# Kernel optimization log

Hardware: AMD Instinct MI355X
Metric: run time of the kernel (lower is better)

Reference implementation:

```python
import jax, jax.numpy as jnp
import numpy as np

FRAME_LENGTH = 2048
HOP_LENGTH = 512


def setup_inputs() -> dict:
    key = jax.random.key(0)
    # (batch, num_channels, samples): 8 clips, stereo, 30 s @ 16 kHz
    x = jax.random.normal(key, (8, 2, 480000), dtype=jnp.float32)
    return {"x": x}


def reference(x):
    """Faithful Enframe.forward.

    The original applies a Conv1d whose weight is the identity matrix
    torch.eye(FL)[:, None, :] with stride=hop, per channel, then concatenates
    channel results along dim=1. Mathematically out[b, n*FL + k, t] =
    x[b, n, t*hop + k]. We implement it as a strided gather (the efficient
    form of the same math).
    """
    B, C, S = x.shape
    FL, HOP = FRAME_LENGTH, HOP_LENGTH
    T = (S - FL) // HOP + 1  # frames_num = 934 for S=480000
    # gather_idx[k, t] = t*HOP + k  -> (FL, T)
    gather_idx = jnp.arange(FL)[:, None] + jnp.arange(T)[None, :] * HOP
    frames = x[:, :, gather_idx]  # (B, C, FL, T)
    # torch.cat over channel dim puts channel-major blocks of size FL on dim 1
    return frames.reshape(B, C * FL, T)
```

## Files before the change

kernel.cpp:

```cpp
#include <hip/hip_runtime.h>


constexpr int FL  = 2048;
constexpr int HOP = 512;
constexpr int TT  = 64;
constexpr int RT  = 64;
constexpr int ROWS = TT + 3;
constexpr int LSTR = RT + 1;

__global__ __launch_bounds__(256)
void enframe_kernel(const float* __restrict__ x, float* __restrict__ out,
                    int S, int T) {
    __shared__ float lds[ROWS * LSTR];

    const int bc = blockIdx.x;
    const int t0 = blockIdx.y * TT;
    const int r0 = blockIdx.z * RT;
    const int tid = threadIdx.x;

    {
        const int rg   = tid & 15;
        const int row0 = tid >> 4;
        const float* xb = x + (size_t)bc * S;
#pragma unroll
        for (int p = 0; p < 5; ++p) {
            const int row = p * 16 + row0;
            if (row < ROWS) {
                const size_t base = (size_t)(t0 + row) * HOP + r0;
                if (base + RT <= (size_t)S) {
                    const float4 v = *(const float4*)(xb + base + rg * 4);
                    float* l = lds + row * LSTR + rg * 4;
                    l[0] = v.x; l[1] = v.y; l[2] = v.z; l[3] = v.w;
                }
            }
        }
    }
    __syncthreads();

    const int tg = tid & 15;
    const int ko = tid >> 4;
    const int tl = tg * 4;
    const int t  = t0 + tl;
    float* ob = out + (size_t)bc * FL * T;
    const bool full = (t + 3 < T);
#pragma unroll
    for (int rb = 0; rb < RT; rb += 16) {
        const int rr = rb + ko;
        const int kb = r0 + rr;
#pragma unroll
        for (int h = 0; h < 4; ++h) {
            const int k = h * HOP + kb;
            const float* l = lds + (tl + h) * LSTR + rr;
            if (full) {
                float4 v = { l[0 * LSTR], l[1 * LSTR], l[2 * LSTR], l[3 * LSTR] };
                *(float4*)(ob + (size_t)k * T + t) = v;
            } else {
#pragma unroll
                for (int j = 0; j < 4; ++j)
                    if (t + j < T) ob[(size_t)k * T + t + j] = l[j * LSTR];
            }
        }
    }
}

extern "C" void kernel_launch(void* const* d_in, const int* in_sizes, int n_in,
                              void* d_out, int out_size, void* d_ws, size_t ws_size,
                              hipStream_t stream) {
    const float* x = (const float*)d_in[0];
    float* out = (float*)d_out;
    const int BC = 16;
    const int S  = in_sizes[0] / BC;
    const int T  = (S - FL) / HOP + 1;
    const int t_tiles = (T + TT - 1) / TT;
    const int r_tiles = HOP / RT;
    dim3 grid(BC, (unsigned)t_tiles, (unsigned)r_tiles);
    enframe_kernel<<<grid, 256, 0, stream>>>(x, out, S, T);
}
```

Before: 152.5 us.

## Loop each block over time chunks with register-prefetched next tile

Restructures the enframe kernel into a persistent-style loop. Each block now handles a 16-row slice of the hop and half of all time chunks, instead of one 64x64 tile. The next chunk's input is prefetched into registers while the current chunk is written out from LDS, overlapping loads with stores. The grid shrinks to 16x32x2 blocks, so fewer blocks are resident, and each thread issues a single narrow 16-float load row. This trades launch parallelism for fewer blocks and less redundant overlap-row loading per tile.

```diff
diff --git a/kernel.cpp b/kernel.cpp
--- a/kernel.cpp
+++ b/kernel.cpp
@@ -1,10 +1,10 @@
 #include <hip/hip_runtime.h>
 
 
-constexpr int FL  = 2048;
-constexpr int HOP = 512;
-constexpr int TT  = 64;
-constexpr int RT  = 64;
+constexpr int FL   = 2048;
+constexpr int HOP  = 512;
+constexpr int RT   = 16;
+constexpr int TT   = 64;
 constexpr int ROWS = TT + 3;
 constexpr int LSTR = RT + 1;
 
@@ -14,50 +14,73 @@
     __shared__ float lds[ROWS * LSTR];
 
     const int bc = blockIdx.x;
-    const int t0 = blockIdx.y * TT;
-    const int r0 = blockIdx.z * RT;
+    const int r0 = blockIdx.y * RT;
+    const int th = blockIdx.z;
+    const int nch  = (T + TT - 1) / TT;
+    const int half = (nch + 1) / 2;
+    const int c_begin = th * half;
+    const int c_end   = th ? nch : half;
+
     const int tid = threadIdx.x;
+    const float* xb = x + (size_t)bc * S;
+    float* ob = out + (size_t)bc * FL * T;
+    const int max_row = S / HOP - 1;
 
+    const int lrow = tid >> 2;
+    const int lrg  = (tid & 3) * 4;
+    const bool tail = tid < (ROWS - 64) * 4;
+    const int trow2 = 64 + (tid >> 2);
+
+    float4 a0 = {0,0,0,0}, a1 = {0,0,0,0};
     {
-        const int rg   = tid & 15;
-        const int row0 = tid >> 4;
-        const float* xb = x + (size_t)bc * S;
-#pragma unroll
-        for (int p = 0; p < 5; ++p) {
-            const int row = p * 16 + row0;
-            if (row < ROWS) {
-                const size_t base = (size_t)(t0 + row) * HOP + r0;
-                if (base + RT <= (size_t)S) {
-                    const float4 v = *(const float4*)(xb + base + rg * 4);
-                    float* l = lds + row * LSTR + rg * 4;
-                    l[0] = v.x; l[1] = v.y; l[2] = v.z; l[3] = v.w;
-                }
+        const int t0 = c_begin * TT;
+        const int tr = t0 + lrow;
+        if (tr <= max_row) a0 = *(const float4*)(xb + (size_t)tr * HOP + r0 + lrg);
+        if (tail) {
+            const int tr2 = t0 + trow2;
+            if (tr2 <= max_row) a1 = *(const float4*)(xb + (size_t)tr2 * HOP + r0 + lrg);
+        }
+    }
+
+    for (int c = c_begin; c < c_end; ++c) {
+        if (c > c_begin) __syncthreads();
+        {
+            float* l = lds + lrow * LSTR + lrg;
+            l[0] = a0.x; l[1] = a0.y; l[2] = a0.z; l[3] = a0.w;
+            if (tail) {
+                float* l2 = lds + trow2 * LSTR + lrg;
+                l2[0] = a1.x; l2[1] = a1.y; l2[2] = a1.z; l2[3] = a1.w;
             }
         }
-    }
-    __syncthreads();
+        __syncthreads();
 
-    const int tg = tid & 15;
-    const int ko = tid >> 4;
-    const int tl = tg * 4;
-    const int t  = t0 + tl;
-    float* ob = out + (size_t)bc * FL * T;
-    const bool full = (t + 3 < T);
-#pragma unroll
-    for (int rb = 0; rb < RT; rb += 16) {
-        const int rr = rb + ko;
-        const int kb = r0 + rr;
+        if (c + 1 < c_end) {
+            const int t0n = (c + 1) * TT;
+            const int tr = t0n + lrow;
+            a0 = (tr <= max_row) ? *(const float4*)(xb + (size_t)tr * HOP + r0 + lrg)
+                                 : float4{0,0,0,0};
+            if (tail) {
+                const int tr2 = t0n + trow2;
+                a1 = (tr2 <= max_row) ? *(const float4*)(xb + (size_t)tr2 * HOP + r0 + lrg)
+                                      : float4{0,0,0,0};
+            }
+        }
+
+        const int t0 = c * TT;
+        const int r  = tid >> 4;
+        const int tl = (tid & 15) * 4;
+        const bool full = (t0 + TT <= T);
 #pragma unroll
         for (int h = 0; h < 4; ++h) {
-            const int k = h * HOP + kb;
-            const float* l = lds + (tl + h) * LSTR + rr;
+            const float* l = lds + (tl + h) * LSTR + r;
+            float* op = ob + (size_t)(h * HOP + r0 + r) * T + t0 + tl;
             if (full) {
-                float4 v = { l[0 * LSTR], l[1 * LSTR], l[2 * LSTR], l[3 * LSTR] };
-                *(float4*)(ob + (size_t)k * T + t) = v;
+                float4 v = { l[0], l[LSTR], l[2 * LSTR], l[3 * LSTR] };
+                *(float4*)op = v;
             } else {
 #pragma unroll
                 for (int j = 0; j < 4; ++j)
-                    if (t + j < T) ob[(size_t)k * T + t + j] = l[j * LSTR];
+                    if (t0 + tl + j < T) op[j] = l[j * LSTR];
             }
         }
     }
@@ -71,8 +94,6 @@
     const int BC = 16;
     const int S  = in_sizes[0] / BC;
     const int T  = (S - FL) / HOP + 1;
-    const int t_tiles = (T + TT - 1) / TT;
-    const int r_tiles = HOP / RT;
-    dim3 grid(BC, (unsigned)t_tiles, (unsigned)r_tiles);
+    dim3 grid(BC, HOP / RT, 2);
     enframe_kernel<<<grid, 256, 0, stream>>>(x, out, S, T);
 }
```

New measurement: 162.0 us. 6.2% more time.
